# Optimization experiments

Measured on AMD Instinct MI355X. Metric: run time of the kernel, lower is better.

Reference implementation:

```python
import jax, jax.numpy as jnp
import numpy as np

HEADS = 4
DIM_HEAD = 32
SCALE = 10.0
EPS = 1e-12  # F.normalize eps


def setup_inputs() -> dict:
    key = jax.random.key(0)
    k0, k1, k2 = jax.random.split(key, 3)
    b, c, h, w = 4, 256, 64, 64
    hidden = HEADS * DIM_HEAD  # 128
    x = jax.random.normal(k0, (b, c, h, w), dtype=jnp.float32)
    # 1x1 convs == per-pixel linear layers; store as [out_ch, in_ch]
    w_qkv = jax.random.normal(k1, (3 * hidden, c), dtype=jnp.float32) * (1.0 / np.sqrt(c))
    w_out = jax.random.normal(k2, (c, hidden), dtype=jnp.float32) * (1.0 / np.sqrt(hidden))
    b_out = jnp.zeros((c,), dtype=jnp.float32)
    return {"x": x, "w_qkv": w_qkv, "w_out": w_out, "b_out": b_out}


def _l2norm(t):
    # normalize along the per-head feature dim d (axis=2 of [b,h,d,n])
    n = jnp.sqrt(jnp.sum(t * t, axis=2, keepdims=True))
    return t / jnp.maximum(n, EPS)


def reference(x, w_qkv, w_out, b_out):
    b, c, h, w = x.shape
    n = h * w
    # to_qkv 1x1 conv (no bias)
    qkv = jnp.einsum('oc,bchw->bohw', w_qkv, x)          # [b, 3*hidden, h, w]
    qkv = qkv.reshape(b, 3, HEADS, DIM_HEAD, n)          # chunk dim=1 then split heads
    q, k, v = qkv[:, 0], qkv[:, 1], qkv[:, 2]            # each [b, heads, d, n]
    q = _l2norm(q)
    k = _l2norm(k)
    sim = jnp.einsum('bhdi,bhdj->bhij', q, k) * SCALE    # [b, heads, n, n]
    attn = jax.nn.softmax(sim, axis=-1)
    out = jnp.einsum('bhij,bhdj->bhid', attn, v)         # [b, heads, n, d]
    # 'b h (x y) d -> b (h d) x y'
    out = out.transpose(0, 1, 3, 2).reshape(b, HEADS * DIM_HEAD, h, w)
    # to_out 1x1 conv with bias
    return jnp.einsum('oc,bchw->bohw', w_out, out) + b_out[None, :, None, None]
```

## Files before the change

### kernel.cpp

```cpp
#include <hip/hip_runtime.h>
#include <math.h>

#define BB 4
#define CC 256
#define NHEAD 4
#define DH 32
#define NN 4096
#define HID 128

typedef _Float16 f16;
typedef _Float16 f16x8 __attribute__((ext_vector_type(8)));
typedef _Float16 f16x4 __attribute__((ext_vector_type(4)));
typedef _Float16 f16x2 __attribute__((ext_vector_type(2)));
typedef float f32x4 __attribute__((ext_vector_type(4)));
typedef unsigned int u32x4 __attribute__((ext_vector_type(4)));

#define QPRESCALE 14.42695041f
#define NSHIFT 14.42695041f

#if __has_builtin(__builtin_amdgcn_exp2f)
#define EXP2F(x) __builtin_amdgcn_exp2f(x)
#else
#define EXP2F(x) __expf((x)*0.6931471805599453f)
#endif

__device__ __forceinline__ f16x8 cvt8(const float* p) {
    float4 a = *(const float4*)p;
    float4 b = *(const float4*)(p + 4);
    f16x8 r;
    r[0] = (f16)a.x; r[1] = (f16)a.y; r[2] = (f16)a.z; r[3] = (f16)a.w;
    r[4] = (f16)b.x; r[5] = (f16)b.y; r[6] = (f16)b.z; r[7] = (f16)b.w;
    return r;
}

__global__ __launch_bounds__(256) void qkv_fused(const float* __restrict__ x,
                                                 const float* __restrict__ wq,
                                                 f16* __restrict__ qh,
                                                 f16* __restrict__ kh,
                                                 f16* __restrict__ vh) {
    int wave = threadIdx.x >> 6, lane = threadIdx.x & 63;
    int quad = lane >> 4, col = lane & 15;
    int b = blockIdx.z;
    int o0 = blockIdx.y * 64;
    int i0 = blockIdx.x * 128 + wave * 32;
    const float* xb = x + (size_t)b * CC * NN;

    f32x4 c[4][2];
#pragma unroll
    for (int mt = 0; mt < 4; mt++)
#pragma unroll
        for (int nt = 0; nt < 2; nt++) c[mt][nt] = f32x4{0.f, 0.f, 0.f, 0.f};

#pragma unroll
    for (int k0 = 0; k0 < CC; k0 += 32) {
        f16x8 a[4];
#pragma unroll
        for (int mt = 0; mt < 4; mt++)
            a[mt] = cvt8(wq + (size_t)(o0 + mt * 16 + col) * CC + k0 + quad * 8);
#pragma unroll
        for (int nt = 0; nt < 2; nt++) {
            const float* xc = xb + (size_t)(k0 + quad * 8) * NN + i0 + nt * 16 + col;
            f16x8 bf;
#pragma unroll
            for (int j = 0; j < 8; j++) bf[j] = (f16)xc[(size_t)j * NN];
#pragma unroll
            for (int mt = 0; mt < 4; mt++)
                c[mt][nt] = __builtin_amdgcn_mfma_f32_16x16x32_f16(a[mt], bf, c[mt][nt], 0, 0, 0);
        }
    }

    if (o0 < 256) {
        int isQ = (o0 < 128);
        int obase = isQ ? o0 : (o0 - 128);
        f16* dst = isQ ? qh : kh;
        float pre = isQ ? QPRESCALE : 1.0f;
#pragma unroll
        for (int nt = 0; nt < 2; nt++) {
#pragma unroll
            for (int hh = 0; hh < 2; hh++) {
                float ss = 0.f;
#pragma unroll
                for (int m2 = 0; m2 < 2; m2++)
#pragma unroll
                    for (int r = 0; r < 4; r++) {
                        float v = c[hh * 2 + m2][nt][r];
                        ss = fmaf(v, v, ss);
                    }
                ss += __shfl_xor(ss, 16);
                ss += __shfl_xor(ss, 32);
                float inv = pre / fmaxf(sqrtf(ss), 1e-12f);
                int h = (obase + hh * 32) >> 5;
                size_t row = ((size_t)(b * 4 + h) * NN + i0 + nt * 16 + col) * 32;
#pragma unroll
                for (int m2 = 0; m2 < 2; m2++) {
                    f16x4 st;
#pragma unroll
                    for (int r = 0; r < 4; r++) st[r] = (f16)(c[hh * 2 + m2][nt][r] * inv);
                    *(f16x4*)(dst + row + m2 * 16 + quad * 4) = st;
                }
            }
        }
    } else {
        int o2 = o0 - 256;
#pragma unroll
        for (int nt = 0; nt < 2; nt++) {
            int i = i0 + nt * 16 + col;
#pragma unroll
            for (int mt = 0; mt < 4; mt++) {
                int h = (o2 + mt * 16) >> 5;
                int d = (mt & 1) * 16 + quad * 4;
#pragma unroll
                for (int r = 0; r < 4; r++)
                    vh[((size_t)(b * 4 + h) * 32 + d + r) * NN + i] = (f16)c[mt][nt][r];
            }
        }
    }
}

#define KROW 40
#define VROW 72

struct G32 {
    f16x8 kA, kB;
    f16x8 v0, v1;
};

__device__ __forceinline__ G32 lds_frags32(const f16* kl, const f16* vl,
                                           int jb, int col, int quad) {
    G32 f;
    f.kA = *(const f16x8*)(kl + (jb + col) * KROW + quad * 8);
    f.kB = *(const f16x8*)(kl + (jb + 16 + col) * KROW + quad * 8);
    f.v0 = *(const f16x8*)(vl + col * VROW + jb + quad * 8);
    f.v1 = *(const f16x8*)(vl + (16 + col) * VROW + jb + quad * 8);
    return f;
}

__device__ __forceinline__ f16x8 expblk2(f32x4 sa, f32x4 sb) {
    u32x4 w;
    w[0] = __builtin_bit_cast(unsigned int,
            __builtin_amdgcn_cvt_pkrtz(EXP2F(sa[0]), EXP2F(sa[1])));
    w[1] = __builtin_bit_cast(unsigned int,
            __builtin_amdgcn_cvt_pkrtz(EXP2F(sa[2]), EXP2F(sa[3])));
    w[2] = __builtin_bit_cast(unsigned int,
            __builtin_amdgcn_cvt_pkrtz(EXP2F(sb[0]), EXP2F(sb[1])));
    w[3] = __builtin_bit_cast(unsigned int,
            __builtin_amdgcn_cvt_pkrtz(EXP2F(sb[2]), EXP2F(sb[3])));
    return __builtin_bit_cast(f16x8, w);
}

__device__ __forceinline__ void compute32g(const G32& f, f16x8 qB0, f16x8 qB1,
                                           f32x4& o00, f32x4& o01,
                                           f32x4& o10, f32x4& o11,
                                           f32x4& lf0, f32x4& lf1) {
    const f32x4 zs = {-NSHIFT, -NSHIFT, -NSHIFT, -NSHIFT};
    f16 one = (f16)1.0f;
    f16x8 ones = {one, one, one, one, one, one, one, one};
    f32x4 sa0 = __builtin_amdgcn_mfma_f32_16x16x32_f16(f.kA, qB0, zs, 0, 0, 0);
    f32x4 sb0 = __builtin_amdgcn_mfma_f32_16x16x32_f16(f.kB, qB0, zs, 0, 0, 0);
    f32x4 sa1 = __builtin_amdgcn_mfma_f32_16x16x32_f16(f.kA, qB1, zs, 0, 0, 0);
    f32x4 sb1 = __builtin_amdgcn_mfma_f32_16x16x32_f16(f.kB, qB1, zs, 0, 0, 0);
    f16x8 p0 = expblk2(sa0, sb0);
    f16x8 p1 = expblk2(sa1, sb1);
    o00 = __builtin_amdgcn_mfma_f32_16x16x32_f16(p0, f.v0, o00, 0, 0, 0);
    o01 = __builtin_amdgcn_mfma_f32_16x16x32_f16(p0, f.v1, o01, 0, 0, 0);
    lf0 = __builtin_amdgcn_mfma_f32_16x16x32_f16(p0, ones, lf0, 0, 0, 0);
    o10 = __builtin_amdgcn_mfma_f32_16x16x32_f16(p1, f.v0, o10, 0, 0, 0);
    o11 = __builtin_amdgcn_mfma_f32_16x16x32_f16(p1, f.v1, o11, 0, 0, 0);
    lf1 = __builtin_amdgcn_mfma_f32_16x16x32_f16(p1, ones, lf1, 0, 0, 0);
}

template <int SPLIT>
__global__ __launch_bounds__(256, 4) void attn_mfma(const f16* __restrict__ qh,
                                                    const f16* __restrict__ kh,
                                                    const f16* __restrict__ vh,
                                                    float* __restrict__ op,
                                                    float* __restrict__ lp,
                                                    f16* __restrict__ att16) {
    __shared__ __align__(16) f16 klds[2][64 * KROW];
    __shared__ __align__(16) f16 vlds[2][32 * VROW];
    int t = threadIdx.x;
    int wave = t >> 6, lane = t & 63;
    int quad = lane >> 4, col = lane & 15;

    int bid = blockIdx.x;
    int xcd = bid & 7;
    int slot = bid >> 3;
    int bh = xcd * 2 + slot / (32 * SPLIT);
    int rem = slot % (32 * SPLIT);
    int s = rem >> 5;
    int i0 = (rem & 31) * 128;
    int iw = i0 + wave * 32;

    const int NT = 64 / SPLIT;
    int kbase = s * (NN / SPLIT);

    const f16* qb = qh + (size_t)bh * NN * 32;
    const f16* kb = kh + (size_t)bh * NN * 32 + (size_t)kbase * 32;
    const f16* vb = vh + (size_t)bh * 32 * NN + kbase;

    f16x8 qB0 = *(const f16x8*)(qb + (size_t)(iw + col) * 32 + quad * 8);
    f16x8 qB1 = *(const f16x8*)(qb + (size_t)(iw + 16 + col) * 32 + quad * 8);

    f32x4 o00 = {0.f, 0.f, 0.f, 0.f}, o01 = o00, o10 = o00, o11 = o00;
    f32x4 lf0 = o00, lf1 = o00;

    int ktr = t >> 2, kts = t & 3;
    int ksrc = (ktr & 32) | ((ktr & 12) << 1) | ((ktr & 16) >> 2) | (ktr & 3);
    int vtr = t >> 3, vts = t & 7;

    f16x8 kr, vr;
    kr = *(const f16x8*)(kb + (size_t)(0 + ksrc) * 32 + kts * 8);
    vr = *(const f16x8*)(vb + (size_t)vtr * NN + 0 + vts * 8);
    *(f16x8*)(&klds[0][0] + ktr * KROW + kts * 8) = kr;
    *(f16x8*)(&vlds[0][0] + vtr * VROW + vts * 8) = vr;
    __syncthreads();
    kr = *(const f16x8*)(kb + (size_t)(64 + ksrc) * 32 + kts * 8);
    vr = *(const f16x8*)(vb + (size_t)vtr * NN + 64 + vts * 8);

    for (int tile = 0; tile < NT - 2; tile++) {
        int buf = tile & 1;
        const f16* kl = &klds[buf][0];
        const f16* vl = &vlds[buf][0];
        G32 g0 = lds_frags32(kl, vl, 0, col, quad);
        G32 g1 = lds_frags32(kl, vl, 32, col, quad);
        compute32g(g0, qB0, qB1, o00, o01, o10, o11, lf0, lf1);
        compute32g(g1, qB0, qB1, o00, o01, o10, o11, lf0, lf1);
        *(f16x8*)(&klds[buf ^ 1][0] + ktr * KROW + kts * 8) = kr;
        *(f16x8*)(&vlds[buf ^ 1][0] + vtr * VROW + vts * 8) = vr;
        __syncthreads();
        int j0 = (tile + 2) * 64;
        kr = *(const f16x8*)(kb + (size_t)(j0 + ksrc) * 32 + kts * 8);
        vr = *(const f16x8*)(vb + (size_t)vtr * NN + j0 + vts * 8);
    }
    {
        G32 g0 = lds_frags32(&klds[0][0], &vlds[0][0], 0, col, quad);
        G32 g1 = lds_frags32(&klds[0][0], &vlds[0][0], 32, col, quad);
        compute32g(g0, qB0, qB1, o00, o01, o10, o11, lf0, lf1);
        compute32g(g1, qB0, qB1, o00, o01, o10, o11, lf0, lf1);
        *(f16x8*)(&klds[1][0] + ktr * KROW + kts * 8) = kr;
        *(f16x8*)(&vlds[1][0] + vtr * VROW + vts * 8) = vr;
        __syncthreads();
    }
    {
        G32 g0 = lds_frags32(&klds[1][0], &vlds[1][0], 0, col, quad);
        G32 g1 = lds_frags32(&klds[1][0], &vlds[1][0], 32, col, quad);
        compute32g(g0, qB0, qB1, o00, o01, o10, o11, lf0, lf1);
        compute32g(g1, qB0, qB1, o00, o01, o10, o11, lf0, lf1);
    }

    if constexpr (SPLIT == 1) {
        int b = bh >> 2, h = bh & 3;
        f16* ab = att16 + (size_t)b * NN * HID + h * 32;
#pragma unroll
        for (int r = 0; r < 4; r++) {
            float inv0 = __builtin_amdgcn_rcpf(lf0[r]);
            float inv1 = __builtin_amdgcn_rcpf(lf1[r]);
            size_t row0 = (size_t)(iw + quad * 4 + r) * HID;
            size_t row1 = (size_t)(iw + 16 + quad * 4 + r) * HID;
            ab[row0 + col]      = (f16)(o00[r] * inv0);
            ab[row0 + 16 + col] = (f16)(o01[r] * inv0);
            ab[row1 + col]      = (f16)(o10[r] * inv1);
            ab[row1 + 16 + col] = (f16)(o11[r] * inv1);
        }
    } else {
        float* ob = op + (size_t)(s * 16 + bh) * NN * 32;
#pragma unroll
        for (int r = 0; r < 4; r++) {
            size_t r0 = (size_t)(iw + quad * 4 + r) * 32;
            size_t r1 = (size_t)(iw + 16 + quad * 4 + r) * 32;
            ob[r0 + col]      = o00[r];
            ob[r0 + 16 + col] = o01[r];
            ob[r1 + col]      = o10[r];
            ob[r1 + 16 + col] = o11[r];
        }
        if (col == 0) {
            float* lb = lp + (size_t)(s * 16 + bh) * NN;
#pragma unroll
            for (int r = 0; r < 4; r++) {
                lb[iw + quad * 4 + r]      = lf0[r];
                lb[iw + 16 + quad * 4 + r] = lf1[r];
            }
        }
    }
}

__global__ __launch_bounds__(256) void attn_combine(const float* __restrict__ op,
                                                    const float* __restrict__ lp,
                                                    f16* __restrict__ att16,
                                                    int nsplit) {
    int gid = blockIdx.x * 256 + threadIdx.x;
    int rowid = gid >> 3;
    int seg = gid & 7;
    int bh = rowid >> 12;
    int q = rowid & 4095;

    float l = 0.f;
    f32x4 acc = {0.f, 0.f, 0.f, 0.f};
    for (int s = 0; s < nsplit; s++) {
        l += lp[(size_t)(s * 16 + bh) * NN + q];
        f32x4 a = *(const f32x4*)(op + ((size_t)(s * 16 + bh) * NN + q) * 32 + seg * 4);
        acc += a;
    }
    float inv = __builtin_amdgcn_rcpf(l);
    int b = bh >> 2, h = bh & 3;
    f16x4 st;
    st[0] = (f16)(acc[0] * inv);
    st[1] = (f16)(acc[1] * inv);
    st[2] = (f16)(acc[2] * inv);
    st[3] = (f16)(acc[3] * inv);
    *(f16x4*)(att16 + ((size_t)b * NN + q) * HID + h * 32 + seg * 4) = st;
}

__global__ __launch_bounds__(256) void out_mfma(const f16* __restrict__ att16,
                                                const float* __restrict__ wo,
                                                const float* __restrict__ bo,
                                                float* __restrict__ out) {
    int wave = threadIdx.x >> 6, lane = threadIdx.x & 63;
    int quad = lane >> 4, col = lane & 15;
    int b = blockIdx.z;
    int i0 = (blockIdx.x * 4 + wave) * 32;
    int o0 = blockIdx.y * 64;
    const f16* ab = att16 + (size_t)b * NN * HID;

    const f32x4 z = {0.f, 0.f, 0.f, 0.f};
    f32x4 c[2][4];
#pragma unroll
    for (int it = 0; it < 2; it++)
#pragma unroll
        for (int ot = 0; ot < 4; ot++) c[it][ot] = z;

#pragma unroll
    for (int k0 = 0; k0 < HID; k0 += 32) {
        f16x8 a0 = *(const f16x8*)(ab + (size_t)(i0 + col) * HID + k0 + quad * 8);
        f16x8 a1 = *(const f16x8*)(ab + (size_t)(i0 + 16 + col) * HID + k0 + quad * 8);
#pragma unroll
        for (int ot = 0; ot < 4; ot++) {
            f16x8 bf = cvt8(wo + (size_t)(o0 + ot * 16 + col) * HID + k0 + quad * 8);
            c[0][ot] = __builtin_amdgcn_mfma_f32_16x16x32_f16(a0, bf, c[0][ot], 0, 0, 0);
            c[1][ot] = __builtin_amdgcn_mfma_f32_16x16x32_f16(a1, bf, c[1][ot], 0, 0, 0);
        }
    }

#pragma unroll
    for (int it = 0; it < 2; it++)
#pragma unroll
        for (int ot = 0; ot < 4; ot++) {
            int o = o0 + ot * 16 + col;
            float bias = bo[o];
            int i = i0 + it * 16 + quad * 4;
            float4 st = {c[it][ot][0] + bias, c[it][ot][1] + bias,
                         c[it][ot][2] + bias, c[it][ot][3] + bias};
            *(float4*)(out + ((size_t)b * CC + o) * NN + i) = st;
        }
}

extern "C" void kernel_launch(void* const* d_in, const int* in_sizes, int n_in,
                              void* d_out, int out_size, void* d_ws, size_t ws_size,
                              hipStream_t stream) {
    const float* x     = (const float*)d_in[0];
    const float* w_qkv = (const float*)d_in[1];
    const float* w_out = (const float*)d_in[2];
    const float* b_out = (const float*)d_in[3];
    float* out = (float*)d_out;

    char* ws = (char*)d_ws;
    f16* qh    = (f16*)(ws);
    f16* kh    = (f16*)(ws + (4u << 20));
    f16* vh    = (f16*)(ws + (8u << 20));
    f16* att16 = (f16*)(ws + (12u << 20));

    qkv_fused<<<dim3(NN / 128, 384 / 64, BB), 256, 0, stream>>>(x, w_qkv, qh, kh, vh);

    if (ws_size >= (50ull << 20)) {
        float* op = (float*)(ws + (16ull << 20));
        float* lp = (float*)(ws + (48ull << 20));
        attn_mfma<4><<<dim3(2048), 256, 0, stream>>>(qh, kh, vh, op, lp, att16);
        attn_combine<<<dim3(2048), 256, 0, stream>>>(op, lp, att16, 4);
    } else if (ws_size >= (33ull << 20)) {
        float* op = (float*)(ws + (16ull << 20));
        float* lp = (float*)(ws + (32ull << 20));
        attn_mfma<2><<<dim3(1024), 256, 0, stream>>>(qh, kh, vh, op, lp, att16);
        attn_combine<<<dim3(2048), 256, 0, stream>>>(op, lp, att16, 2);
    } else {
        attn_mfma<1><<<dim3(512), 256, 0, stream>>>(qh, kh, vh, nullptr, nullptr, att16);
    }

    out_mfma<<<dim3(NN / 128, CC / 64, BB), 256, 0, stream>>>(att16, w_out, b_out, out);
}
```

Baseline: 158.6 us.

## Process 64 query rows per wave to reuse K/V LDS fragments

Each wave now handles four 16-row query fragments (64 rows) instead of two, so each block covers 256 queries and the grid is halved. Every K/V fragment loaded from LDS feeds twice as many MFMAs, which cuts LDS read traffic and the number of global K/V tile loads per query. The cost is more accumulator and query registers per thread, which may lower occupancy under the 4-blocks launch bound, and fewer blocks (1024 with the default split) to fill the GPU.

```diff
diff --git a/kernel.cpp b/kernel.cpp
--- a/kernel.cpp
+++ b/kernel.cpp
@@ -11,7 +11,6 @@
 typedef _Float16 f16;
 typedef _Float16 f16x8 __attribute__((ext_vector_type(8)));
 typedef _Float16 f16x4 __attribute__((ext_vector_type(4)));
-typedef _Float16 f16x2 __attribute__((ext_vector_type(2)));
 typedef float f32x4 __attribute__((ext_vector_type(4)));
 typedef unsigned int u32x4 __attribute__((ext_vector_type(4)));
 
@@ -120,21 +119,6 @@
 #define KROW 40
 #define VROW 72
 
-struct G32 {
-    f16x8 kA, kB;
-    f16x8 v0, v1;
-};
-
-__device__ __forceinline__ G32 lds_frags32(const f16* kl, const f16* vl,
-                                           int jb, int col, int quad) {
-    G32 f;
-    f.kA = *(const f16x8*)(kl + (jb + col) * KROW + quad * 8);
-    f.kB = *(const f16x8*)(kl + (jb + 16 + col) * KROW + quad * 8);
-    f.v0 = *(const f16x8*)(vl + col * VROW + jb + quad * 8);
-    f.v1 = *(const f16x8*)(vl + (16 + col) * VROW + jb + quad * 8);
-    return f;
-}
-
 __device__ __forceinline__ f16x8 expblk2(f32x4 sa, f32x4 sb) {
     u32x4 w;
     w[0] = __builtin_bit_cast(unsigned int,
@@ -148,25 +132,25 @@
     return __builtin_bit_cast(f16x8, w);
 }
 
-__device__ __forceinline__ void compute32g(const G32& f, f16x8 qB0, f16x8 qB1,
-                                           f32x4& o00, f32x4& o01,
-                                           f32x4& o10, f32x4& o11,
-                                           f32x4& lf0, f32x4& lf1) {
+__device__ __forceinline__ void compute_g(const f16* kl, const f16* vl, int jb,
+                                          int col, int quad, const f16x8 (&qB)[4],
+                                          f32x4 (&o)[4][2], f32x4 (&lf)[4]) {
+    f16x8 kA = *(const f16x8*)(kl + (jb + col) * KROW + quad * 8);
+    f16x8 kB = *(const f16x8*)(kl + (jb + 16 + col) * KROW + quad * 8);
+    f16x8 v0 = *(const f16x8*)(vl + col * VROW + jb + quad * 8);
+    f16x8 v1 = *(const f16x8*)(vl + (16 + col) * VROW + jb + quad * 8);
     const f32x4 zs = {-NSHIFT, -NSHIFT, -NSHIFT, -NSHIFT};
     f16 one = (f16)1.0f;
     f16x8 ones = {one, one, one, one, one, one, one, one};
-    f32x4 sa0 = __builtin_amdgcn_mfma_f32_16x16x32_f16(f.kA, qB0, zs, 0, 0, 0);
-    f32x4 sb0 = __builtin_amdgcn_mfma_f32_16x16x32_f16(f.kB, qB0, zs, 0, 0, 0);
-    f32x4 sa1 = __builtin_amdgcn_mfma_f32_16x16x32_f16(f.kA, qB1, zs, 0, 0, 0);
-    f32x4 sb1 = __builtin_amdgcn_mfma_f32_16x16x32_f16(f.kB, qB1, zs, 0, 0, 0);
-    f16x8 p0 = expblk2(sa0, sb0);
-    f16x8 p1 = expblk2(sa1, sb1);
-    o00 = __builtin_amdgcn_mfma_f32_16x16x32_f16(p0, f.v0, o00, 0, 0, 0);
-    o01 = __builtin_amdgcn_mfma_f32_16x16x32_f16(p0, f.v1, o01, 0, 0, 0);
-    lf0 = __builtin_amdgcn_mfma_f32_16x16x32_f16(p0, ones, lf0, 0, 0, 0);
-    o10 = __builtin_amdgcn_mfma_f32_16x16x32_f16(p1, f.v0, o10, 0, 0, 0);
-    o11 = __builtin_amdgcn_mfma_f32_16x16x32_f16(p1, f.v1, o11, 0, 0, 0);
-    lf1 = __builtin_amdgcn_mfma_f32_16x16x32_f16(p1, ones, lf1, 0, 0, 0);
+#pragma unroll
+    for (int f = 0; f < 4; f++) {
+        f32x4 sa = __builtin_amdgcn_mfma_f32_16x16x32_f16(kA, qB[f], zs, 0, 0, 0);
+        f32x4 sb = __builtin_amdgcn_mfma_f32_16x16x32_f16(kB, qB[f], zs, 0, 0, 0);
+        f16x8 p = expblk2(sa, sb);
+        o[f][0] = __builtin_amdgcn_mfma_f32_16x16x32_f16(p, v0, o[f][0], 0, 0, 0);
+        o[f][1] = __builtin_amdgcn_mfma_f32_16x16x32_f16(p, v1, o[f][1], 0, 0, 0);
+        lf[f]   = __builtin_amdgcn_mfma_f32_16x16x32_f16(p, ones, lf[f], 0, 0, 0);
+    }
 }
 
 template <int SPLIT>
@@ -185,11 +169,11 @@
     int bid = blockIdx.x;
     int xcd = bid & 7;
     int slot = bid >> 3;
-    int bh = xcd * 2 + slot / (32 * SPLIT);
-    int rem = slot % (32 * SPLIT);
-    int s = rem >> 5;
-    int i0 = (rem & 31) * 128;
-    int iw = i0 + wave * 32;
+    int bh = xcd * 2 + slot / (16 * SPLIT);
+    int rem = slot % (16 * SPLIT);
+    int s = rem >> 4;
+    int i0 = (rem & 15) * 256;
+    int iw = i0 + wave * 64;
 
     const int NT = 64 / SPLIT;
     int kbase = s * (NN / SPLIT);
@@ -198,11 +182,18 @@
     const f16* kb = kh + (size_t)bh * NN * 32 + (size_t)kbase * 32;
     const f16* vb = vh + (size_t)bh * 32 * NN + kbase;
 
-    f16x8 qB0 = *(const f16x8*)(qb + (size_t)(iw + col) * 32 + quad * 8);
-    f16x8 qB1 = *(const f16x8*)(qb + (size_t)(iw + 16 + col) * 32 + quad * 8);
-
-    f32x4 o00 = {0.f, 0.f, 0.f, 0.f}, o01 = o00, o10 = o00, o11 = o00;
-    f32x4 lf0 = o00, lf1 = o00;
+    f16x8 qB[4];
+#pragma unroll
+    for (int f = 0; f < 4; f++)
+        qB[f] = *(const f16x8*)(qb + (size_t)(iw + f * 16 + col) * 32 + quad * 8);
+
+    f32x4 o[4][2], lf[4];
+#pragma unroll
+    for (int f = 0; f < 4; f++) {
+        o[f][0] = f32x4{0.f, 0.f, 0.f, 0.f};
+        o[f][1] = f32x4{0.f, 0.f, 0.f, 0.f};
+        lf[f]   = f32x4{0.f, 0.f, 0.f, 0.f};
+    }
 
     int ktr = t >> 2, kts = t & 3;
     int ksrc = (ktr & 32) | ((ktr & 12) << 1) | ((ktr & 16) >> 2) | (ktr & 3);
@@ -221,10 +212,8 @@
         int buf = tile & 1;
         const f16* kl = &klds[buf][0];
         const f16* vl = &vlds[buf][0];
-        G32 g0 = lds_frags32(kl, vl, 0, col, quad);
-        G32 g1 = lds_frags32(kl, vl, 32, col, quad);
-        compute32g(g0, qB0, qB1, o00, o01, o10, o11, lf0, lf1);
-        compute32g(g1, qB0, qB1, o00, o01, o10, o11, lf0, lf1);
+        compute_g(kl, vl, 0, col, quad, qB, o, lf);
+        compute_g(kl, vl, 32, col, quad, qB, o, lf);
         *(f16x8*)(&klds[buf ^ 1][0] + ktr * KROW + kts * 8) = kr;
         *(f16x8*)(&vlds[buf ^ 1][0] + vtr * VROW + vts * 8) = vr;
         __syncthreads();
@@ -233,53 +222,46 @@
         vr = *(const f16x8*)(vb + (size_t)vtr * NN + j0 + vts * 8);
     }
     {
-        G32 g0 = lds_frags32(&klds[0][0], &vlds[0][0], 0, col, quad);
-        G32 g1 = lds_frags32(&klds[0][0], &vlds[0][0], 32, col, quad);
-        compute32g(g0, qB0, qB1, o00, o01, o10, o11, lf0, lf1);
-        compute32g(g1, qB0, qB1, o00, o01, o10, o11, lf0, lf1);
+        compute_g(&klds[0][0], &vlds[0][0], 0, col, quad, qB, o, lf);
+        compute_g(&klds[0][0], &vlds[0][0], 32, col, quad, qB, o, lf);
         *(f16x8*)(&klds[1][0] + ktr * KROW + kts * 8) = kr;
         *(f16x8*)(&vlds[1][0] + vtr * VROW + vts * 8) = vr;
         __syncthreads();
     }
     {
-        G32 g0 = lds_frags32(&klds[1][0], &vlds[1][0], 0, col, quad);
-        G32 g1 = lds_frags32(&klds[1][0], &vlds[1][0], 32, col, quad);
-        compute32g(g0, qB0, qB1, o00, o01, o10, o11, lf0, lf1);
-        compute32g(g1, qB0, qB1, o00, o01, o10, o11, lf0, lf1);
+        compute_g(&klds[1][0], &vlds[1][0], 0, col, quad, qB, o, lf);
+        compute_g(&klds[1][0], &vlds[1][0], 32, col, quad, qB, o, lf);
     }
 
     if constexpr (SPLIT == 1) {
         int b = bh >> 2, h = bh & 3;
         f16* ab = att16 + (size_t)b * NN * HID + h * 32;
 #pragma unroll
-        for (int r = 0; r < 4; r++) {
-            float inv0 = __builtin_amdgcn_rcpf(lf0[r]);
-            float inv1 = __builtin_amdgcn_rcpf(lf1[r]);
-            size_t row0 = (size_t)(iw + quad * 4 + r) * HID;
-            size_t row1 = (size_t)(iw + 16 + quad * 4 + r) * HID;
-            ab[row0 + col]      = (f16)(o00[r] * inv0);
-            ab[row0 + 16 + col] = (f16)(o01[r] * inv0);
-            ab[row1 + col]      = (f16)(o10[r] * inv1);
-            ab[row1 + 16 + col] = (f16)(o11[r] * inv1);
-        }
+        for (int f = 0; f < 4; f++)
+#pragma unroll
+            for (int r = 0; r < 4; r++) {
+                float inv = __builtin_amdgcn_rcpf(lf[f][r]);
+                size_t row = (size_t)(iw + f * 16 + quad * 4 + r) * HID;
+                ab[row + col]      = (f16)(o[f][0][r] * inv);
+                ab[row + 16 + col] = (f16)(o[f][1][r] * inv);
+            }
     } else {
         float* ob = op + (size_t)(s * 16 + bh) * NN * 32;
 #pragma unroll
-        for (int r = 0; r < 4; r++) {
-            size_t r0 = (size_t)(iw + quad * 4 + r) * 32;
-            size_t r1 = (size_t)(iw + 16 + quad * 4 + r) * 32;
-            ob[r0 + col]      = o00[r];
-            ob[r0 + 16 + col] = o01[r];
-            ob[r1 + col]      = o10[r];
-            ob[r1 + 16 + col] = o11[r];
-        }
+        for (int f = 0; f < 4; f++)
+#pragma unroll
+            for (int r = 0; r < 4; r++) {
+                size_t rr = (size_t)(iw + f * 16 + quad * 4 + r) * 32;
+                ob[rr + col]      = o[f][0][r];
+                ob[rr + 16 + col] = o[f][1][r];
+            }
         if (col == 0) {
             float* lb = lp + (size_t)(s * 16 + bh) * NN;
 #pragma unroll
-            for (int r = 0; r < 4; r++) {
-                lb[iw + quad * 4 + r]      = lf0[r];
-                lb[iw + 16 + quad * 4 + r] = lf1[r];
-            }
+            for (int f = 0; f < 4; f++)
+#pragma unroll
+                for (int r = 0; r < 4; r++)
+                    lb[iw + f * 16 + quad * 4 + r] = lf[f][r];
         }
     }
 }
@@ -374,15 +356,15 @@
     if (ws_size >= (50ull << 20)) {
         float* op = (float*)(ws + (16ull << 20));
         float* lp = (float*)(ws + (48ull << 20));
-        attn_mfma<4><<<dim3(2048), 256, 0, stream>>>(qh, kh, vh, op, lp, att16);
+        attn_mfma<4><<<dim3(1024), 256, 0, stream>>>(qh, kh, vh, op, lp, att16);
         attn_combine<<<dim3(2048), 256, 0, stream>>>(op, lp, att16, 4);
     } else if (ws_size >= (33ull << 20)) {
         float* op = (float*)(ws + (16ull << 20));
         float* lp = (float*)(ws + (32ull << 20));
-        attn_mfma<2><<<dim3(1024), 256, 0, stream>>>(qh, kh, vh, op, lp, att16);
+        attn_mfma<2><<<dim3(512), 256, 0, stream>>>(qh, kh, vh, op, lp, att16);
         attn_combine<<<dim3(2048), 256, 0, stream>>>(op, lp, att16, 2);
     } else {
-        attn_mfma<1><<<dim3(512), 256, 0, stream>>>(qh, kh, vh, nullptr, nullptr, att16);
+        attn_mfma<1><<<dim3(256), 256, 0, stream>>>(qh, kh, vh, nullptr, nullptr, att16);
     }
 
     out_mfma<<<dim3(NN / 128, CC / 64, BB), 256, 0, stream>>>(att16, w_out, b_out, out);
```

Result: faster. 155.0 us (-2.3%).
